# Kernel optimization log

Hardware: AMD Instinct MI355X
Metric: run time of the kernel (lower is better)

The kernel has to match this reference:

```python
import jax, jax.numpy as jnp
import numpy as np

B, T, C = 64, 256, 64
E, H, HB, OUT = 32, 64, 128, 2


def setup_inputs() -> dict:
    key = jax.random.key(0)
    ks = iter(jax.random.split(key, 32))
    s = 0.02
    p = {}
    p["x"] = jax.random.normal(next(ks), (B, T, C), jnp.float32)
    # embedding Linear(1, E)
    p["embed_w"] = jax.random.normal(next(ks), (E, 1), jnp.float32) * s
    p["embed_b"] = jnp.zeros((E,), jnp.float32)
    # GRU (input E, hidden H); gate order r,z,n
    p["w_ih"] = jax.random.normal(next(ks), (3 * H, E), jnp.float32) * s
    p["w_hh"] = jax.random.normal(next(ks), (3 * H, H), jnp.float32) * s
    p["b_ih"] = jnp.zeros((3 * H,), jnp.float32)
    p["b_hh"] = jnp.zeros((3 * H,), jnp.float32)
    # BTP query / key MLPs: H->HB->HB->HB
    for nm in ("q", "k"):
        p[f"{nm}1_w"] = jax.random.normal(next(ks), (HB, H), jnp.float32) * s
        p[f"{nm}1_b"] = jnp.zeros((HB,), jnp.float32)
        p[f"{nm}2_w"] = jax.random.normal(next(ks), (HB, HB), jnp.float32) * s
        p[f"{nm}2_b"] = jnp.zeros((HB,), jnp.float32)
        p[f"{nm}3_w"] = jax.random.normal(next(ks), (HB, HB), jnp.float32) * s
        p[f"{nm}3_b"] = jnp.zeros((HB,), jnp.float32)
    # Gate bias (n_components x n_components), torch.randn init
    p["gate_bias"] = jax.random.normal(next(ks), (C, C), jnp.float32)
    # classifier: C^2 -> C^2/2 -> C^2/4 -> OUT
    d0, d1, d2 = C * C, C * C // 2, C * C // 4
    p["clf1_w"] = jax.random.normal(next(ks), (d1, d0), jnp.float32) * s
    p["clf1_b"] = jnp.zeros((d1,), jnp.float32)
    p["clf2_w"] = jax.random.normal(next(ks), (d2, d1), jnp.float32) * s
    p["clf2_b"] = jnp.zeros((d2,), jnp.float32)
    p["clf3_w"] = jax.random.normal(next(ks), (OUT, d2), jnp.float32) * s
    p["clf3_b"] = jnp.zeros((OUT,), jnp.float32)
    # predictor Linear(H, 1)
    p["pred_w"] = jax.random.normal(next(ks), (1, H), jnp.float32) * s
    p["pred_b"] = jnp.zeros((1,), jnp.float32)
    return p


def _mlp3(h, w1, b1, w2, b2, w3, b3):
    h = jax.nn.relu(h @ w1.T + b1)
    h = jax.nn.relu(h @ w2.T + b2)
    return h @ w3.T + b3


def reference(x, embed_w, embed_b, w_ih, w_hh, b_ih, b_hh,
              q1_w, q1_b, q2_w, q2_b, q3_w, q3_b,
              k1_w, k1_b, k2_w, k2_b, k3_w, k3_b,
              gate_bias, clf1_w, clf1_b, clf2_w, clf2_b, clf3_w, clf3_b,
              pred_w, pred_b):
    Bb, Tt, Cc = x.shape
    Hh = w_hh.shape[1]
    # embeddings: Linear(1,E) applied to each scalar -> [B,C,T,E]
    embedded = x.transpose(0, 2, 1)[..., None] * embed_w[:, 0] + embed_b
    xs = jnp.moveaxis(embedded, 2, 0)  # [T,B,C,E]

    def gru_cell(h, xt):
        gi = xt @ w_ih.T + b_ih           # [B,C,3H]
        gh = h @ w_hh.T + b_hh
        gi_r, gi_z, gi_n = jnp.split(gi, 3, axis=-1)
        gh_r, gh_z, gh_n = jnp.split(gh, 3, axis=-1)
        r = jax.nn.sigmoid(gi_r + gh_r)
        z = jax.nn.sigmoid(gi_z + gh_z)
        n = jnp.tanh(gi_n + r * gh_n)
        return (1.0 - z) * n + z * h

    def btp(h):
        q = _mlp3(h, q1_w, q1_b, q2_w, q2_b, q3_w, q3_b)   # [B,C,HB]
        k = _mlp3(h, k1_w, k1_b, k2_w, k2_b, k3_w, k3_b)
        transfer = jnp.einsum('bqd,bkd->bqk', q, k)        # [B,C,C]
        norms = jnp.sqrt(jnp.sum(transfer * transfer, axis=(1, 2), keepdims=True))
        transfer = transfer / norms
        gate = jax.nn.sigmoid(jnp.abs(transfer) + gate_bias)
        transfer = transfer * gate
        next_states = jnp.einsum('bij,bjd->bid', transfer, h)
        return next_states, transfer

    def step(h, xt):
        h = gru_cell(h, xt)
        h, transfer = btp(h)
        return h, (h, transfer)

    h0 = jnp.zeros((Bb, Cc, Hh), x.dtype)
    _, (hs, mats) = jax.lax.scan(step, h0, xs)
    hidden_states = jnp.moveaxis(hs, 0, 1)    # [B,T,C,H]
    matrices = jnp.moveaxis(mats, 0, 1)       # [B,T,C,C]

    # predictor on hidden states at t=0..T-2 -> predicts x[:,1:,:]
    predicted = (hidden_states[:, :-1] @ pred_w.T + pred_b)[..., 0]  # [B,T-1,C]

    clf_in = matrices.reshape(Bb, Tt, Cc * Cc)
    h1 = jax.nn.relu(clf_in @ clf1_w.T + clf1_b)   # dropout is identity in eval
    h2 = jax.nn.relu(h1 @ clf2_w.T + clf2_b)
    time_logits = h2 @ clf3_w.T + clf3_b            # [B,T,OUT]
    logits = jnp.mean(time_logits, axis=1)          # [B,OUT]
    return logits, matrices, time_logits, predicted, x[:, 1:, :]
```

## Files before the change

kernel.cpp:

```cpp
#include <hip/hip_runtime.h>
#include <hip/hip_bf16.h>
#include <math.h>

#define B_BATCH 64
#define T_STEPS 256
#define C_COMP  64

#define WSW_BYTE_OFF 2048
#define WHH_OFF 0
#define Q1_OFF 12288
#define K1_OFF 20480
#define Q2_OFF 28672
#define K2_OFF 45056
#define Q3_OFF 61440
#define K3_OFF 77824
#define C1WB_BYTE 262144
#define C2WB_BYTE 17039360
#define H1B_BYTE  21233664
#define H2B_BYTE  88342528
#define MB16_BYTE 121896960ULL

#define MAT_OFF  128
#define TL_OFF   67108992
#define PRED_OFF 67141760
#define XC_OFF   68186240

typedef __attribute__((ext_vector_type(8))) short short8;
typedef __attribute__((ext_vector_type(4))) float f32x4;
#define MFMA16(a,b,c) __builtin_amdgcn_mfma_f32_16x16x32_bf16(a,b,c,0,0,0)

__device__ __forceinline__ float fsigm(float v) {
    return __builtin_amdgcn_rcpf(1.0f + __expf(-v));
}
__device__ __forceinline__ float ftanh(float v) {
    return 1.0f - 2.0f * __builtin_amdgcn_rcpf(__expf(2.0f * v) + 1.0f);
}
__device__ __forceinline__ short f2bs(float f) {
    unsigned u = __float_as_uint(f);
    u += 0x7fffu + ((u >> 16) & 1u);
    return (short)(u >> 16);
}
__device__ __forceinline__ float bf2f(short s) {
    return __uint_as_float(((unsigned)(unsigned short)s) << 16);
}
__device__ __forceinline__ void bar_lds() {
    asm volatile("s_waitcnt lgkmcnt(0)" ::: "memory");
    __builtin_amdgcn_s_barrier();
}
__device__ __forceinline__ int swz64(int row, int col) {
    return row * 64 + (col ^ (((row >> 1) & 7) << 3));
}
__device__ __forceinline__ int swz128(int row, int col) {
    return row * 128 + (col ^ (((row >> 1) & 7) << 3));
}
__device__ __forceinline__ void async16(void* lds, const void* g) {
    __builtin_amdgcn_global_load_lds((const __attribute__((address_space(1))) void*)g,
                                     (__attribute__((address_space(3))) void*)lds, 16, 0, 0);
}

__global__ void precompute_kernel(const float* __restrict__ w_ih,
                                  const float* __restrict__ embed_w,
                                  const float* __restrict__ embed_b,
                                  const float* __restrict__ b_ih,
                                  float* __restrict__ avec, float* __restrict__ cvec)
{
    int g = threadIdx.x;
    if (g < 192) {
        float a = 0.f, c = 0.f;
        for (int e = 0; e < 32; ++e) {
            float w = w_ih[g * 32 + e];
            a += w * embed_w[e];
            c += w * embed_b[e];
        }
        avec[g] = a;
        cvec[g] = c + b_ih[g];
    }
}

__global__ void tobf16_kernel(const float* __restrict__ src, short* __restrict__ dst, int n)
{
    int i = blockIdx.x * 256 + threadIdx.x;
    if (i < n) dst[i] = f2bs(src[i]);
}

__global__ void expand_kernel(const short* __restrict__ mb, float* __restrict__ mat)
{
    const size_t i = ((size_t)blockIdx.x * 256 + threadIdx.x) * 8;
    short8 v = *(const short8*)&mb[i];
    float4 lo, hi;
    lo.x = bf2f(v[0]); lo.y = bf2f(v[1]); lo.z = bf2f(v[2]); lo.w = bf2f(v[3]);
    hi.x = bf2f(v[4]); hi.y = bf2f(v[5]); hi.z = bf2f(v[6]); hi.w = bf2f(v[7]);
    *reinterpret_cast<float4*>(&mat[i])     = lo;
    *reinterpret_cast<float4*>(&mat[i + 4]) = hi;
}

template<int KST, int AST, bool RELU>
__device__ __forceinline__ void two_strip(
    const short* __restrict__ A,
    const short8* __restrict__ B0, const short8* __restrict__ B1,
    const float bias0, const float bias1,
    short* __restrict__ outb, const int s0, const int s1, const int ln, const int lh)
{
    f32x4 acc0[4], acc1[4];
#pragma unroll
    for (int m = 0; m < 4; ++m) {
        acc0[m] = (f32x4){bias0, bias0, bias0, bias0};
        acc1[m] = (f32x4){bias1, bias1, bias1, bias1};
    }
#pragma unroll
    for (int kk = 0; kk < KST; ++kk)
#pragma unroll
        for (int m = 0; m < 4; ++m) {
            const int row = m * 16 + ln;
            short8 a = *(const short8*)&A[row * AST + ((kk * 32 + lh * 8) ^ (((row >> 1) & 7) << 3))];
            acc0[m] = MFMA16(a, B0[kk], acc0[m]);
            acc1[m] = MFMA16(a, B1[kk], acc1[m]);
        }
#pragma unroll
    for (int m = 0; m < 4; ++m)
#pragma unroll
        for (int q = 0; q < 4; ++q) {
            const int row = m * 16 + lh * 4 + q;
            float v0 = acc0[m][q], v1 = acc1[m][q];
            if (RELU) { v0 = fmaxf(v0, 0.f); v1 = fmaxf(v1, 0.f); }
            outb[swz128(row, s0 * 16 + ln)] = f2bs(v0);
            outb[swz128(row, s1 * 16 + ln)] = f2bs(v1);
        }
}

__global__ __launch_bounds__(512) void scan_kernel(
    const float* __restrict__ x, const float* __restrict__ b_hh,
    const float* __restrict__ avec, const float* __restrict__ cvec,
    const short* __restrict__ wsw,
    const float* __restrict__ q1b, const float* __restrict__ q2b, const float* __restrict__ q3b,
    const float* __restrict__ k1b, const float* __restrict__ k2b, const float* __restrict__ k3b,
    const float* __restrict__ gate_bias,
    const float* __restrict__ pred_w, const float* __restrict__ pred_b,
    float* __restrict__ matrices, float* __restrict__ predicted,
    short* __restrict__ mb16, const int use_mb16)
{
    __shared__ __align__(16) float h32[64 * 65];
    __shared__ __align__(16) short hb [64 * 64];
    __shared__ __align__(16) short hbT[64 * 64];
    __shared__ __align__(16) short qf [64 * 128];
    __shared__ __align__(16) short kf [64 * 128];
    __shared__ __align__(16) float gbias_s[64 * 65];
    __shared__ __align__(16) char arena[65536];
    __shared__ float avec_s[192], cvec_s[192], bhh_s[192], pw_s[64], xrow[64], red[8];

    float* gates = (float*)arena;
    short* act1q = (short*)arena;
    short* act1k = (short*)(arena + 16384);
    short* act2q = (short*)(arena + 32768);
    short* act2k = (short*)(arena + 49152);
    float* tf    = (float*)arena;

    const int tid = threadIdx.x;
    const int b = blockIdx.x;
    const int w = tid >> 6, lane = tid & 63;
    const int ln = lane & 15, lh = lane >> 4;
    const int path = w >> 2;
    const int wq = w & 3;

    for (int i = tid; i < 64 * 65; i += 512) h32[i] = 0.f;
    for (int i = tid; i < 64 * 64; i += 512) { hb[i] = 0; hbT[i] = 0; }
    for (int i = tid; i < 4096; i += 512)
        gbias_s[(i >> 6) * 65 + (i & 63)] = gate_bias[i];
    if (tid < 192) { avec_s[tid] = avec[tid]; cvec_s[tid] = cvec[tid]; bhh_s[tid] = b_hh[tid]; }
    if (tid < 64) pw_s[tid] = pred_w[tid];
    const float pbv = pred_b[0];

    const short* whh_b = wsw + WHH_OFF;
    const short* l1w = path ? wsw + K1_OFF : wsw + Q1_OFF;
    const short* l2w = path ? wsw + K2_OFF : wsw + Q2_OFF;
    const short* l3w = path ? wsw + K3_OFF : wsw + Q3_OFF;
    const float* l1b = path ? k1b : q1b;
    const float* l2b = path ? k2b : q2b;
    const float* l3b = path ? k3b : q3b;

    short8 Bg[2][2], B1[2][2], B2[2][4], B3[2][4];
    {
        const int sg1 = (w < 4) ? (w + 8) : w;
#pragma unroll
        for (int kk = 0; kk < 2; ++kk) {
            Bg[0][kk] = *(const short8*)&whh_b[(w   * 16 + ln) * 64 + kk * 32 + lh * 8];
            Bg[1][kk] = *(const short8*)&whh_b[(sg1 * 16 + ln) * 64 + kk * 32 + lh * 8];
        }
#pragma unroll
        for (int s = 0; s < 2; ++s) {
            const int strip = wq + s * 4;
#pragma unroll
            for (int kk = 0; kk < 2; ++kk)
                B1[s][kk] = *(const short8*)&l1w[(strip * 16 + ln) * 64 + kk * 32 + lh * 8];
#pragma unroll
            for (int kk = 0; kk < 4; ++kk) {
                B2[s][kk] = *(const short8*)&l2w[(strip * 16 + ln) * 128 + kk * 32 + lh * 8];
                B3[s][kk] = *(const short8*)&l3w[(strip * 16 + ln) * 128 + kk * 32 + lh * 8];
            }
        }
    }
    const float b1v0 = l1b[wq * 16 + ln],     b1v1 = l1b[(wq + 4) * 16 + ln];
    const float b2v0 = l2b[wq * 16 + ln],     b2v1 = l2b[(wq + 4) * 16 + ln];
    const float b3v0 = l3b[wq * 16 + ln],     b3v1 = l3b[(wq + 4) * 16 + ln];
    __syncthreads();

    for (int t = 0; t < T_STEPS; ++t) {
        float xpre = 0.f;
        if (tid < 64) xpre = x[((size_t)b * T_STEPS + t) * 64 + tid];
        if (t > 0) {
            const int c = tid >> 3, jj = tid & 7;
            float p = 0.f;
#pragma unroll
            for (int u = 0; u < 8; ++u) p = fmaf(h32[c * 65 + jj * 8 + u], pw_s[jj * 8 + u], p);
            p += __shfl_xor(p, 1); p += __shfl_xor(p, 2); p += __shfl_xor(p, 4);
            if (jj == 0) predicted[((size_t)b * (T_STEPS - 1) + (t - 1)) * 64 + c] = p + pbv;
        }
        {
            f32x4 a0[4], a1[4];
#pragma unroll
            for (int m = 0; m < 4; ++m) { a0[m] = (f32x4){0,0,0,0}; a1[m] = (f32x4){0,0,0,0}; }
#pragma unroll
            for (int kk = 0; kk < 2; ++kk)
#pragma unroll
                for (int m = 0; m < 4; ++m) {
                    short8 av = *(const short8*)&hb[swz64(m * 16 + ln, kk * 32 + lh * 8)];
                    a0[m] = MFMA16(av, Bg[0][kk], a0[m]);
                    a1[m] = MFMA16(av, Bg[1][kk], a1[m]);
                }
#pragma unroll
            for (int m = 0; m < 4; ++m)
#pragma unroll
                for (int q = 0; q < 4; ++q)
                    gates[(m * 16 + lh * 4 + q) * 193 + w * 16 + ln] = a0[m][q];
            if (w < 4) {
#pragma unroll
                for (int m = 0; m < 4; ++m)
#pragma unroll
                    for (int q = 0; q < 4; ++q)
                        gates[(m * 16 + lh * 4 + q) * 193 + (w + 8) * 16 + ln] = a1[m][q];
            }
        }
        if (tid < 64) xrow[tid] = xpre;
        bar_lds();

        {
            const int c = tid >> 3, j0 = (tid & 7) * 8;
            const float xv = xrow[c];
            short8 hv8;
#pragma unroll
            for (int jj = 0; jj < 8; ++jj) {
                const int j = j0 + jj;
                const float ghr = gates[c * 193 + j]       + bhh_s[j];
                const float ghz = gates[c * 193 + 64 + j]  + bhh_s[64 + j];
                const float ghn = gates[c * 193 + 128 + j] + bhh_s[128 + j];
                const float r = fsigm(fmaf(xv, avec_s[j],        cvec_s[j])        + ghr);
                const float z = fsigm(fmaf(xv, avec_s[64 + j],   cvec_s[64 + j])   + ghz);
                const float n = ftanh(fmaf(xv, avec_s[128 + j], cvec_s[128 + j]) + r * ghn);
                const float hold = h32[c * 65 + j];
                const float hn = fmaf(z, hold - n, n);
                h32[c * 65 + j] = hn;
                const short hv = f2bs(hn);
                hv8[jj] = hv;
                hbT[swz64(j, c)] = hv;
            }
            *(short8*)&hb[c * 64 + (j0 ^ (((c >> 1) & 7) << 3))] = hv8;
        }
        bar_lds();

        two_strip<2, 64,  true >(hb, B1[0], B1[1], b1v0, b1v1,
                                 path ? act1k : act1q, wq, wq + 4, ln, lh);
        bar_lds();
        two_strip<4, 128, true >(path ? act1k : act1q, B2[0], B2[1], b2v0, b2v1,
                                 path ? act2k : act2q, wq, wq + 4, ln, lh);
        bar_lds();
        two_strip<4, 128, false>(path ? act2k : act2q, B3[0], B3[1], b3v0, b3v1,
                                 path ? kf : qf, wq, wq + 4, ln, lh);
        bar_lds();

        {
            const int m = wq, n0 = w >> 2;
            f32x4 ac0 = {0,0,0,0}, ac1 = {0,0,0,0};
#pragma unroll
            for (int kk = 0; kk < 4; ++kk) {
                short8 a  = *(const short8*)&qf[swz128(m * 16 + ln, kk * 32 + lh * 8)];
                short8 b0 = *(const short8*)&kf[swz128(n0 * 16 + ln, kk * 32 + lh * 8)];
                short8 b1 = *(const short8*)&kf[swz128((n0 + 2) * 16 + ln, kk * 32 + lh * 8)];
                ac0 = MFMA16(a, b0, ac0);
                ac1 = MFMA16(a, b1, ac1);
            }
            float ss = 0.f;
#pragma unroll
            for (int q = 0; q < 4; ++q) {
                const int row = m * 16 + lh * 4 + q;
                tf[row * 65 + n0 * 16 + ln]       = ac0[q];
                tf[row * 65 + (n0 + 2) * 16 + ln] = ac1[q];
                ss = fmaf(ac0[q], ac0[q], fmaf(ac1[q], ac1[q], ss));
            }
#pragma unroll
            for (int off = 1; off < 64; off <<= 1) ss += __shfl_xor(ss, off);
            if (lane == 0) red[w] = ss;
        }
        bar_lds();

        {
            const int m = wq, n0 = w >> 2;
            const float ssum = red[0]+red[1]+red[2]+red[3]+red[4]+red[5]+red[6]+red[7];
            const float inv = __builtin_amdgcn_rsqf(ssum);
            const int row = m * 16 + ln;
            short8 af[2];
            float vals[16];
#pragma unroll
            for (int kk = 0; kk < 2; ++kk)
#pragma unroll
                for (int u = 0; u < 8; ++u) {
                    const int col = kk * 32 + lh * 8 + u;
                    const float tv = tf[row * 65 + col] * inv;
                    const float g = fsigm(fabsf(tv) + gbias_s[row * 65 + col]);
                    const float v = tv * g;
                    vals[kk * 8 + u] = v;
                    af[kk][u] = f2bs(v);
                }
            const size_t mbase = ((size_t)b * T_STEPS + t) * 4096;
            if (w < 4) {
                if (use_mb16) {
#pragma unroll
                    for (int kk = 0; kk < 2; ++kk)
                        *(short8*)&mb16[mbase + row * 64 + kk * 32 + lh * 8] = af[kk];
                } else {
#pragma unroll
                    for (int kk = 0; kk < 2; ++kk) {
                        float4 lo = {vals[kk*8+0], vals[kk*8+1], vals[kk*8+2], vals[kk*8+3]};
                        float4 hi = {vals[kk*8+4], vals[kk*8+5], vals[kk*8+6], vals[kk*8+7]};
                        *reinterpret_cast<float4*>(&matrices[mbase + row * 64 + kk * 32 + lh * 8])     = lo;
                        *reinterpret_cast<float4*>(&matrices[mbase + row * 64 + kk * 32 + lh * 8 + 4]) = hi;
                    }
                }
            }
            f32x4 hc0 = {0,0,0,0}, hc1 = {0,0,0,0};
#pragma unroll
            for (int kk = 0; kk < 2; ++kk) {
                short8 b0 = *(const short8*)&hbT[swz64(n0 * 16 + ln, kk * 32 + lh * 8)];
                short8 b1 = *(const short8*)&hbT[swz64((n0 + 2) * 16 + ln, kk * 32 + lh * 8)];
                hc0 = MFMA16(af[kk], b0, hc0);
                hc1 = MFMA16(af[kk], b1, hc1);
            }
#pragma unroll
            for (int q = 0; q < 4; ++q) {
                const int orow = m * 16 + lh * 4 + q;
                const int c0 = n0 * 16 + ln, c1 = (n0 + 2) * 16 + ln;
                h32[orow * 65 + c0] = hc0[q];
                h32[orow * 65 + c1] = hc1[q];
                hb[swz64(orow, c0)] = f2bs(hc0[q]);
                hb[swz64(orow, c1)] = f2bs(hc1[q]);
            }
        }
        bar_lds();
    }
}

__global__ void copyx_kernel(const float* __restrict__ x, float* __restrict__ out5)
{
    int i = blockIdx.x * 256 + threadIdx.x;
    if (i < B_BATCH * (T_STEPS - 1) * C_COMP) {
        int b = i / ((T_STEPS - 1) * C_COMP);
        int r = i - b * (T_STEPS - 1) * C_COMP;
        out5[i] = x[(size_t)b * (T_STEPS * C_COMP) + r + C_COMP];
    }
}

__global__ __launch_bounds__(256) void gemm1_kernel(
    const float* __restrict__ A, const short* __restrict__ Bw,
    const float* __restrict__ bias, short* __restrict__ Cb,
    const int M, const int N, const int K)
{
    __shared__ __align__(16) short Asb[128 * 64];
    __shared__ __align__(16) short Bsb[128 * 64];
    const int tid = threadIdx.x;
    const int w = tid >> 6, lane = tid & 63;
    const int ln = lane & 15, lh = lane >> 4;
    const int wr = w >> 1, wc = w & 1;

    const int ntc = N >> 7;
    const int g = blockIdx.x;
    const int xcd = g & 7, chunk = g >> 3;
    const int mt = xcd * ((M >> 7) >> 3) + chunk / ntc;
    const int nt = chunk % ntc;
    const int m0 = mt << 7, n0 = nt << 7;

    const int ar = tid >> 1;
    const int ac = (tid & 1) << 5;
    const short* bsrc = Bw + (size_t)(n0 + w * 32 + (lane >> 3)) * K + ((lane & 7) << 3);
    short* bdst = &Bsb[w * 32 * 64 + lane * 8];

    f32x4 acc[4][4];
#pragma unroll
    for (int m = 0; m < 4; ++m)
#pragma unroll
        for (int n = 0; n < 4; ++n) acc[m][n] = (f32x4){0, 0, 0, 0};

    for (int k0 = 0; k0 < K; k0 += 64) {
        const float* arow = A + (size_t)(m0 + ar) * K + k0 + ac;
        float4 av[8];
#pragma unroll
        for (int i = 0; i < 8; ++i) av[i] = *reinterpret_cast<const float4*>(arow + i * 4);
        short8 cv[4];
#pragma unroll
        for (int i = 0; i < 4; ++i) {
            cv[i][0] = f2bs(av[2*i].x);   cv[i][1] = f2bs(av[2*i].y);
            cv[i][2] = f2bs(av[2*i].z);   cv[i][3] = f2bs(av[2*i].w);
            cv[i][4] = f2bs(av[2*i+1].x); cv[i][5] = f2bs(av[2*i+1].y);
            cv[i][6] = f2bs(av[2*i+1].z); cv[i][7] = f2bs(av[2*i+1].w);
        }
        __syncthreads();
#pragma unroll
        for (int i = 0; i < 4; ++i)
            *reinterpret_cast<short8*>(&Asb[ar * 64 + ac + i * 8]) = cv[i];
#pragma unroll
        for (int i = 0; i < 4; ++i)
            async16(bdst + i * 512, bsrc + (size_t)i * 8 * K + k0);
        __syncthreads();
#pragma unroll
        for (int kk = 0; kk < 2; ++kk) {
            short8 af[4], bfr[4];
#pragma unroll
            for (int m = 0; m < 4; ++m)
                af[m] = *reinterpret_cast<const short8*>(&Asb[(wr*64 + m*16 + ln)*64 + kk*32 + lh*8]);
#pragma unroll
            for (int n = 0; n < 4; ++n)
                bfr[n] = *reinterpret_cast<const short8*>(&Bsb[(wc*64 + n*16 + ln)*64 + kk*32 + lh*8]);
#pragma unroll
            for (int m = 0; m < 4; ++m)
#pragma unroll
                for (int n = 0; n < 4; ++n)
                    acc[m][n] = MFMA16(af[m], bfr[n], acc[m][n]);
        }
    }
#pragma unroll
    for (int n = 0; n < 4; ++n) {
        const int col = n0 + wc * 64 + n * 16 + ln;
        const float bv = bias[col];
#pragma unroll
        for (int m = 0; m < 4; ++m)
#pragma unroll
            for (int q = 0; q < 4; ++q) {
                const int row = m0 + wr * 64 + m * 16 + lh * 4 + q;
                Cb[(size_t)row * N + col] = f2bs(fmaxf(acc[m][n][q] + bv, 0.f));
            }
    }
}

__global__ __launch_bounds__(256) void gemm2_kernel(
    const short* __restrict__ Ab, const short* __restrict__ Bw,
    const float* __restrict__ bias, short* __restrict__ Cb,
    const int M, const int N, const int K)
{
    __shared__ __align__(16) short Asb[128 * 64];
    __shared__ __align__(16) short Bsb[128 * 64];
    const int tid = threadIdx.x;
    const int w = tid >> 6, lane = tid & 63;
    const int ln = lane & 15, lh = lane >> 4;
    const int wr = w >> 1, wc = w & 1;

    const int ntc = N >> 7;
    const int g = blockIdx.x;
    const int xcd = g & 7, chunk = g >> 3;
    const int mt = xcd * ((M >> 7) >> 3) + chunk / ntc;
    const int nt = chunk % ntc;
    const int m0 = mt << 7, n0 = nt << 7;

    const short* asrc = Ab + (size_t)(m0 + w * 32 + (lane >> 3)) * K + ((lane & 7) << 3);
    const short* bsrc = Bw + (size_t)(n0 + w * 32 + (lane >> 3)) * K + ((lane & 7) << 3);
    short* adst = &Asb[w * 32 * 64 + lane * 8];
    short* bdst = &Bsb[w * 32 * 64 + lane * 8];

    f32x4 acc[4][4];
#pragma unroll
    for (int m = 0; m < 4; ++m)
#pragma unroll
        for (int n = 0; n < 4; ++n) acc[m][n] = (f32x4){0, 0, 0, 0};

    for (int k0 = 0; k0 < K; k0 += 64) {
        __syncthreads();
#pragma unroll
        for (int i = 0; i < 4; ++i) {
            async16(adst + i * 512, asrc + (size_t)i * 8 * K + k0);
            async16(bdst + i * 512, bsrc + (size_t)i * 8 * K + k0);
        }
        __syncthreads();
#pragma unroll
        for (int kk = 0; kk < 2; ++kk) {
            short8 af[4], bfr[4];
#pragma unroll
            for (int m = 0; m < 4; ++m)
                af[m] = *reinterpret_cast<const short8*>(&Asb[(wr*64 + m*16 + ln)*64 + kk*32 + lh*8]);
#pragma unroll
            for (int n = 0; n < 4; ++n)
                bfr[n] = *reinterpret_cast<const short8*>(&Bsb[(wc*64 + n*16 + ln)*64 + kk*32 + lh*8]);
#pragma unroll
            for (int m = 0; m < 4; ++m)
#pragma unroll
                for (int n = 0; n < 4; ++n)
                    acc[m][n] = MFMA16(af[m], bfr[n], acc[m][n]);
        }
    }
#pragma unroll
    for (int n = 0; n < 4; ++n) {
        const int col = n0 + wc * 64 + n * 16 + ln;
        const float bv = bias[col];
#pragma unroll
        for (int m = 0; m < 4; ++m)
#pragma unroll
            for (int q = 0; q < 4; ++q) {
                const int row = m0 + wr * 64 + m * 16 + lh * 4 + q;
                Cb[(size_t)row * N + col] = f2bs(fmaxf(acc[m][n][q] + bv, 0.f));
            }
    }
}

__global__ __launch_bounds__(256) void clf3_kernel(const short* __restrict__ h2b,
    const float* __restrict__ w3, const float* __restrict__ b3, float* __restrict__ TL)
{
    const int lane = threadIdx.x & 63;
    const int w = threadIdx.x >> 6;
    const size_t r = (size_t)blockIdx.x * 4 + w;
    const short* hr = h2b + r * 1024;
    float a0 = 0.f, a1 = 0.f;
#pragma unroll
    for (int half = 0; half < 2; ++half) {
        const int k = half * 512 + lane * 8;
        short8 hv = *(const short8*)&hr[k];
#pragma unroll
        for (int u = 0; u < 8; ++u) {
            const float hf = bf2f(hv[u]);
            a0 = fmaf(hf, w3[k + u], a0);
            a1 = fmaf(hf, w3[1024 + k + u], a1);
        }
    }
    for (int off = 32; off; off >>= 1) { a0 += __shfl_xor(a0, off); a1 += __shfl_xor(a1, off); }
    if (lane == 0) {
        TL[r * 2 + 0] = a0 + b3[0];
        TL[r * 2 + 1] = a1 + b3[1];
    }
}

__global__ void logits_kernel(const float* __restrict__ TL, float* __restrict__ out)
{
    const int tid = threadIdx.x;
    if (tid >= 128) return;
    const int b = tid >> 1, o = tid & 1;
    float s = 0.f;
    for (int t = 0; t < T_STEPS; ++t) s += TL[((size_t)b * T_STEPS + t) * 2 + o];
    out[b * 2 + o] = s * (1.0f / 256.0f);
}

extern "C" void kernel_launch(void* const* d_in, const int* in_sizes, int n_in,
                              void* d_out, int out_size, void* d_ws, size_t ws_size,
                              hipStream_t stream)
{
    const float* x       = (const float*)d_in[0];
    const float* embed_w = (const float*)d_in[1];
    const float* embed_b = (const float*)d_in[2];
    const float* w_ih    = (const float*)d_in[3];
    const float* w_hh    = (const float*)d_in[4];
    const float* b_ih    = (const float*)d_in[5];
    const float* b_hh    = (const float*)d_in[6];
    const float* q1w = (const float*)d_in[7],  *q1b = (const float*)d_in[8];
    const float* q2w = (const float*)d_in[9],  *q2b = (const float*)d_in[10];
    const float* q3w = (const float*)d_in[11], *q3b = (const float*)d_in[12];
    const float* k1w = (const float*)d_in[13], *k1b = (const float*)d_in[14];
    const float* k2w = (const float*)d_in[15], *k2b = (const float*)d_in[16];
    const float* k3w = (const float*)d_in[17], *k3b = (const float*)d_in[18];
    const float* gate_bias = (const float*)d_in[19];
    const float* c1w = (const float*)d_in[20], *c1b = (const float*)d_in[21];
    const float* c2w = (const float*)d_in[22], *c2b = (const float*)d_in[23];
    const float* c3w = (const float*)d_in[24], *c3b = (const float*)d_in[25];
    const float* pw  = (const float*)d_in[26], *pb  = (const float*)d_in[27];

    float* out       = (float*)d_out;
    float* logits    = out;
    float* matrices  = out + MAT_OFF;
    float* TL        = out + TL_OFF;
    float* predicted = out + PRED_OFF;
    float* xcopy     = out + XC_OFF;

    float* ws   = (float*)d_ws;
    float* avec = ws;
    float* cvec = ws + 192;
    short* wsw  = (short*)((char*)d_ws + WSW_BYTE_OFF);
    short* c1wb = (short*)((char*)d_ws + C1WB_BYTE);
    short* c2wb = (short*)((char*)d_ws + C2WB_BYTE);
    short* h1b  = (short*)((char*)d_ws + H1B_BYTE);
    short* h2b  = (short*)((char*)d_ws + H2B_BYTE);

    const int use_mb16 = (ws_size >= MB16_BYTE + 134217728ULL) ? 1 : 0;
    short* mb16 = use_mb16 ? (short*)((char*)d_ws + MB16_BYTE) : (short*)d_ws;

    precompute_kernel<<<1, 256, 0, stream>>>(w_ih, embed_w, embed_b, b_ih, avec, cvec);

    tobf16_kernel<<<(12288 + 255) / 256, 256, 0, stream>>>(w_hh, wsw + WHH_OFF, 12288);
    tobf16_kernel<<<(8192  + 255) / 256, 256, 0, stream>>>(q1w,  wsw + Q1_OFF,  8192);
    tobf16_kernel<<<(8192  + 255) / 256, 256, 0, stream>>>(k1w,  wsw + K1_OFF,  8192);
    tobf16_kernel<<<(16384 + 255) / 256, 256, 0, stream>>>(q2w,  wsw + Q2_OFF,  16384);
    tobf16_kernel<<<(16384 + 255) / 256, 256, 0, stream>>>(k2w,  wsw + K2_OFF,  16384);
    tobf16_kernel<<<(16384 + 255) / 256, 256, 0, stream>>>(q3w,  wsw + Q3_OFF,  16384);
    tobf16_kernel<<<(16384 + 255) / 256, 256, 0, stream>>>(k3w,  wsw + K3_OFF,  16384);
    tobf16_kernel<<<(2048 * 4096 + 255) / 256, 256, 0, stream>>>(c1w, c1wb, 2048 * 4096);
    tobf16_kernel<<<(1024 * 2048 + 255) / 256, 256, 0, stream>>>(c2w, c2wb, 1024 * 2048);

    scan_kernel<<<B_BATCH, 512, 0, stream>>>(x, b_hh, avec, cvec, wsw,
        q1b, q2b, q3b, k1b, k2b, k3b, gate_bias, pw, pb, matrices, predicted,
        mb16, use_mb16);

    if (use_mb16)
        expand_kernel<<<32768, 256, 0, stream>>>(mb16, matrices);

    copyx_kernel<<<(B_BATCH * (T_STEPS - 1) * C_COMP + 255) / 256, 256, 0, stream>>>(x, xcopy);

    const int Mtot = B_BATCH * T_STEPS;
    if (use_mb16) {
        gemm2_kernel<<<(Mtot / 128) * (2048 / 128), 256, 0, stream>>>(
            mb16, c1wb, c1b, h1b, Mtot, 2048, 4096);
    } else {
        gemm1_kernel<<<(Mtot / 128) * (2048 / 128), 256, 0, stream>>>(
            matrices, c1wb, c1b, h1b, Mtot, 2048, 4096);
    }
    gemm2_kernel<<<(Mtot / 128) * (1024 / 128), 256, 0, stream>>>(
        h1b, c2wb, c2b, h2b, Mtot, 1024, 2048);
    clf3_kernel<<<Mtot / 4, 256, 0, stream>>>(h2b, c3w, c3b, TL);
    logits_kernel<<<1, 128, 0, stream>>>(TL, logits);
}
```

Measured before the change: 3.250 ms.

## Fuse GRU gate matmul with elementwise update in registers, drop gates LDS round-trip

Each wave now computes all three gate outputs (r, z, n) for its own 16-column slice and two 16-row blocks, so the GRU nonlinearity runs straight from MFMA accumulators. This removes the gates staging buffer in LDS and one barrier per timestep. The new state is written to a separate buffer that feeds the query/key MLP. The fp32 hidden state is dropped; the old state, the predictor input and the recurrence now all read bf16 copies, which lowers precision. The x row for the next step is prefetched a step ahead, and biases and vectors are kept in registers.

```diff
diff --git a/kernel.cpp b/kernel.cpp
--- a/kernel.cpp
+++ b/kernel.cpp
@@ -26,6 +26,7 @@
 #define XC_OFF   68186240
 
 typedef __attribute__((ext_vector_type(8))) short short8;
+typedef __attribute__((ext_vector_type(4))) short short4v;
 typedef __attribute__((ext_vector_type(4))) float f32x4;
 #define MFMA16(a,b,c) __builtin_amdgcn_mfma_f32_16x16x32_bf16(a,b,c,0,0,0)
 
@@ -139,16 +140,16 @@
     float* __restrict__ matrices, float* __restrict__ predicted,
     short* __restrict__ mb16, const int use_mb16)
 {
-    __shared__ __align__(16) float h32[64 * 65];
-    __shared__ __align__(16) short hb [64 * 64];
-    __shared__ __align__(16) short hbT[64 * 64];
-    __shared__ __align__(16) short qf [64 * 128];
-    __shared__ __align__(16) short kf [64 * 128];
+    __shared__ __align__(16) short hb  [64 * 64];
+    __shared__ __align__(16) short hbN [64 * 64];
+    __shared__ __align__(16) short hbT [64 * 64];
+    __shared__ __align__(16) short hbP [64 * 72];
+    __shared__ __align__(16) short qf  [64 * 128];
+    __shared__ __align__(16) short kf  [64 * 128];
     __shared__ __align__(16) float gbias_s[64 * 65];
     __shared__ __align__(16) char arena[65536];
-    __shared__ float avec_s[192], cvec_s[192], bhh_s[192], pw_s[64], xrow[64], red[8];
-
-    float* gates = (float*)arena;
+    __shared__ float xrow[64], pw_s[64], red[8];
+
     short* act1q = (short*)arena;
     short* act1k = (short*)(arena + 16384);
     short* act2q = (short*)(arena + 32768);
@@ -161,14 +162,20 @@
     const int ln = lane & 15, lh = lane >> 4;
     const int path = w >> 2;
     const int wq = w & 3;
-
-    for (int i = tid; i < 64 * 65; i += 512) h32[i] = 0.f;
-    for (int i = tid; i < 64 * 64; i += 512) { hb[i] = 0; hbT[i] = 0; }
+    const int jg = w & 3;
+    const int mb = (w >> 2) * 2;
+
+    for (int i = tid; i < 64 * 64; i += 512) { hb[i] = 0; hbN[i] = 0; hbT[i] = 0; }
+    for (int i = tid; i < 64 * 72; i += 512) hbP[i] = 0;
     for (int i = tid; i < 4096; i += 512)
         gbias_s[(i >> 6) * 65 + (i & 63)] = gate_bias[i];
-    if (tid < 192) { avec_s[tid] = avec[tid]; cvec_s[tid] = cvec[tid]; bhh_s[tid] = b_hh[tid]; }
-    if (tid < 64) pw_s[tid] = pred_w[tid];
+    if (tid < 64) { pw_s[tid] = pred_w[tid]; xrow[tid] = x[(size_t)b * T_STEPS * 64 + tid]; }
     const float pbv = pred_b[0];
+
+    const int jlane = jg * 16 + ln;
+    const float bhh_r = b_hh[jlane],       bhh_z = b_hh[64 + jlane],  bhh_n = b_hh[128 + jlane];
+    const float av_r  = avec[jlane],       av_z  = avec[64 + jlane],  av_n  = avec[128 + jlane];
+    const float cv_r  = cvec[jlane],       cv_z  = cvec[64 + jlane],  cv_n  = cvec[128 + jlane];
 
     const short* whh_b = wsw + WHH_OFF;
     const short* l1w = path ? wsw + K1_OFF : wsw + Q1_OFF;
@@ -178,25 +185,24 @@
     const float* l2b = path ? k2b : q2b;
     const float* l3b = path ? k3b : q3b;
 
-    short8 Bg[2][2], B1[2][2], B2[2][4], B3[2][4];
-    {
-        const int sg1 = (w < 4) ? (w + 8) : w;
-#pragma unroll
-        for (int kk = 0; kk < 2; ++kk) {
-            Bg[0][kk] = *(const short8*)&whh_b[(w   * 16 + ln) * 64 + kk * 32 + lh * 8];
-            Bg[1][kk] = *(const short8*)&whh_b[(sg1 * 16 + ln) * 64 + kk * 32 + lh * 8];
-        }
-#pragma unroll
-        for (int s = 0; s < 2; ++s) {
-            const int strip = wq + s * 4;
-#pragma unroll
-            for (int kk = 0; kk < 2; ++kk)
-                B1[s][kk] = *(const short8*)&l1w[(strip * 16 + ln) * 64 + kk * 32 + lh * 8];
-#pragma unroll
-            for (int kk = 0; kk < 4; ++kk) {
-                B2[s][kk] = *(const short8*)&l2w[(strip * 16 + ln) * 128 + kk * 32 + lh * 8];
-                B3[s][kk] = *(const short8*)&l3w[(strip * 16 + ln) * 128 + kk * 32 + lh * 8];
-            }
+    short8 Bg[3][2];
+#pragma unroll
+    for (int g = 0; g < 3; ++g)
+#pragma unroll
+        for (int kk = 0; kk < 2; ++kk)
+            Bg[g][kk] = *(const short8*)&whh_b[(g * 64 + jg * 16 + ln) * 64 + kk * 32 + lh * 8];
+
+    short8 B1[2][2], B2[2][4], B3[2][4];
+#pragma unroll
+    for (int s = 0; s < 2; ++s) {
+        const int strip = wq + s * 4;
+#pragma unroll
+        for (int kk = 0; kk < 2; ++kk)
+            B1[s][kk] = *(const short8*)&l1w[(strip * 16 + ln) * 64 + kk * 32 + lh * 8];
+#pragma unroll
+        for (int kk = 0; kk < 4; ++kk) {
+            B2[s][kk] = *(const short8*)&l2w[(strip * 16 + ln) * 128 + kk * 32 + lh * 8];
+            B3[s][kk] = *(const short8*)&l3w[(strip * 16 + ln) * 128 + kk * 32 + lh * 8];
         }
     }
     const float b1v0 = l1b[wq * 16 + ln],     b1v1 = l1b[(wq + 4) * 16 + ln];
@@ -205,69 +211,62 @@
     __syncthreads();
 
     for (int t = 0; t < T_STEPS; ++t) {
-        float xpre = 0.f;
-        if (tid < 64) xpre = x[((size_t)b * T_STEPS + t) * 64 + tid];
+        float xnext = 0.f;
+        if (tid < 64 && t + 1 < T_STEPS)
+            xnext = x[((size_t)b * T_STEPS + t + 1) * 64 + tid];
+
         if (t > 0) {
-            const int c = tid >> 3, jj = tid & 7;
+            const int r = w * 8 + (lane >> 3);
+            const int seg = (lane & 7) * 8;
+            short8 hv = *(const short8*)&hbP[r * 72 + seg];
             float p = 0.f;
 #pragma unroll
-            for (int u = 0; u < 8; ++u) p = fmaf(h32[c * 65 + jj * 8 + u], pw_s[jj * 8 + u], p);
+            for (int u = 0; u < 8; ++u) p = fmaf(bf2f(hv[u]), pw_s[seg + u], p);
             p += __shfl_xor(p, 1); p += __shfl_xor(p, 2); p += __shfl_xor(p, 4);
-            if (jj == 0) predicted[((size_t)b * (T_STEPS - 1) + (t - 1)) * 64 + c] = p + pbv;
+            if ((lane & 7) == 0)
+                predicted[((size_t)b * (T_STEPS - 1) + (t - 1)) * 64 + r] = p + pbv;
         }
         {
-            f32x4 a0[4], a1[4];
-#pragma unroll
-            for (int m = 0; m < 4; ++m) { a0[m] = (f32x4){0,0,0,0}; a1[m] = (f32x4){0,0,0,0}; }
+            f32x4 accG[3][2];
+#pragma unroll
+            for (int g = 0; g < 3; ++g) {
+                const float bi = (g == 0) ? bhh_r : (g == 1) ? bhh_z : bhh_n;
+#pragma unroll
+                for (int mm = 0; mm < 2; ++mm) accG[g][mm] = (f32x4){bi, bi, bi, bi};
+            }
 #pragma unroll
             for (int kk = 0; kk < 2; ++kk)
 #pragma unroll
-                for (int m = 0; m < 4; ++m) {
-                    short8 av = *(const short8*)&hb[swz64(m * 16 + ln, kk * 32 + lh * 8)];
-                    a0[m] = MFMA16(av, Bg[0][kk], a0[m]);
-                    a1[m] = MFMA16(av, Bg[1][kk], a1[m]);
+                for (int mm = 0; mm < 2; ++mm) {
+                    short8 a = *(const short8*)&hb[swz64((mb + mm) * 16 + ln, kk * 32 + lh * 8)];
+#pragma unroll
+                    for (int g = 0; g < 3; ++g)
+                        accG[g][mm] = MFMA16(a, Bg[g][kk], accG[g][mm]);
                 }
 #pragma unroll
-            for (int m = 0; m < 4; ++m)
-#pragma unroll
-                for (int q = 0; q < 4; ++q)
-                    gates[(m * 16 + lh * 4 + q) * 193 + w * 16 + ln] = a0[m][q];
-            if (w < 4) {
-#pragma unroll
-                for (int m = 0; m < 4; ++m)
-#pragma unroll
-                    for (int q = 0; q < 4; ++q)
-                        gates[(m * 16 + lh * 4 + q) * 193 + (w + 8) * 16 + ln] = a1[m][q];
-            }
-        }
-        if (tid < 64) xrow[tid] = xpre;
+            for (int mm = 0; mm < 2; ++mm) {
+                short hq[4];
+#pragma unroll
+                for (int q = 0; q < 4; ++q) {
+                    const int c = (mb + mm) * 16 + lh * 4 + q;
+                    const float xv = xrow[c];
+                    const float hold = bf2f(hb[c * 64 + (jlane ^ (((c >> 1) & 7) << 3))]);
+                    const float r = fsigm(accG[0][mm][q] + fmaf(xv, av_r, cv_r));
+                    const float z = fsigm(accG[1][mm][q] + fmaf(xv, av_z, cv_z));
+                    const float n = ftanh(fmaf(r, accG[2][mm][q], fmaf(xv, av_n, cv_n)));
+                    const float hn = fmaf(z, hold - n, n);
+                    const short hv = f2bs(hn);
+                    hq[q] = hv;
+                    hbN[c * 64 + (jlane ^ (((c >> 1) & 7) << 3))] = hv;
+                }
+                short4v t4; t4[0] = hq[0]; t4[1] = hq[1]; t4[2] = hq[2]; t4[3] = hq[3];
+                const int tcol = (mb + mm) * 16 + lh * 4;
+                *(short4v*)&hbT[jlane * 64 + (tcol ^ (((jlane >> 1) & 7) << 3))] = t4;
+            }
+        }
         bar_lds();
 
-        {
-            const int c = tid >> 3, j0 = (tid & 7) * 8;
-            const float xv = xrow[c];
-            short8 hv8;
-#pragma unroll
-            for (int jj = 0; jj < 8; ++jj) {
-                const int j = j0 + jj;
-                const float ghr = gates[c * 193 + j]       + bhh_s[j];
-                const float ghz = gates[c * 193 + 64 + j]  + bhh_s[64 + j];
-                const float ghn = gates[c * 193 + 128 + j] + bhh_s[128 + j];
-                const float r = fsigm(fmaf(xv, avec_s[j],        cvec_s[j])        + ghr);
-                const float z = fsigm(fmaf(xv, avec_s[64 + j],   cvec_s[64 + j])   + ghz);
-                const float n = ftanh(fmaf(xv, avec_s[128 + j], cvec_s[128 + j]) + r * ghn);
-                const float hold = h32[c * 65 + j];
-                const float hn = fmaf(z, hold - n, n);
-                h32[c * 65 + j] = hn;
-                const short hv = f2bs(hn);
-                hv8[jj] = hv;
-                hbT[swz64(j, c)] = hv;
-            }
-            *(short8*)&hb[c * 64 + (j0 ^ (((c >> 1) & 7) << 3))] = hv8;
-        }
-        bar_lds();
-
-        two_strip<2, 64,  true >(hb, B1[0], B1[1], b1v0, b1v1,
+        two_strip<2, 64,  true >(hbN, B1[0], B1[1], b1v0, b1v1,
                                  path ? act1k : act1q, wq, wq + 4, ln, lh);
         bar_lds();
         two_strip<4, 128, true >(path ? act1k : act1q, B2[0], B2[1], b2v0, b2v1,
@@ -299,6 +298,7 @@
 #pragma unroll
             for (int off = 1; off < 64; off <<= 1) ss += __shfl_xor(ss, off);
             if (lane == 0) red[w] = ss;
+            if (tid < 64 && t + 1 < T_STEPS) xrow[tid] = xnext;
         }
         bar_lds();
 
@@ -348,10 +348,11 @@
             for (int q = 0; q < 4; ++q) {
                 const int orow = m * 16 + lh * 4 + q;
                 const int c0 = n0 * 16 + ln, c1 = (n0 + 2) * 16 + ln;
-                h32[orow * 65 + c0] = hc0[q];
-                h32[orow * 65 + c1] = hc1[q];
-                hb[swz64(orow, c0)] = f2bs(hc0[q]);
-                hb[swz64(orow, c1)] = f2bs(hc1[q]);
+                const short v0 = f2bs(hc0[q]), v1 = f2bs(hc1[q]);
+                hb[swz64(orow, c0)] = v0;
+                hb[swz64(orow, c1)] = v1;
+                hbP[orow * 72 + c0] = v0;
+                hbP[orow * 72 + c1] = v1;
             }
         }
         bar_lds();
```

After: 3.739 ms. 1.15x slower.
